# Performance work log

Hardware: AMD Instinct MI355X
Metric: run time of the kernel (lower is better)

The kernel has to match this reference:

```python
import jax, jax.numpy as jnp
import numpy as np

LEFT = 5
RIGHT = 5

def setup_inputs() -> dict:
    key = jax.random.key(0)
    k1, k2 = jax.random.split(key)
    x = jax.random.normal(k1, (32, 2000, 80), dtype=jnp.float32)
    lengths = jax.random.uniform(k2, (32,), dtype=jnp.float32)
    return {"x": x, "lengths": lengths}

def reference(x, lengths):
    # x: [B, T, C]. The torch module's grouped conv1d with a one-hot eye kernel
    # is exactly a sliding-window gather: output channel (c, i) at time t equals
    # x[t + i - LEFT, c] with zero padding outside [0, T).
    B, T, C = x.shape
    ctx_len = LEFT + RIGHT + 1
    x_pad = jnp.pad(x, ((0, 0), (LEFT, RIGHT), (0, 0)))  # [B, T+L+R, C]
    # stack shifted views: ctx[b, t, c, i] = x[t + i - LEFT, c]
    ctx = jnp.stack([x_pad[:, i:i + T, :] for i in range(ctx_len)], axis=-1)  # [B,T,C,ctx_len]
    # torch conv output channel order is channel-major (c fastest over ctx index)
    cw_x = ctx.reshape(B, T, C * ctx_len)
    # length masking: len_abs = round(T * lengths); mask[b, t] = t < len_abs[b]
    len_abs = jnp.round(T * lengths).astype(jnp.int32)
    mask = (jnp.arange(T)[None, :] < len_abs[:, None]).astype(cw_x.dtype)  # [B, T]
    return cw_x * mask[:, :, None]
```

## Files before the change

kernel.cpp:

```cpp
#include <hip/hip_runtime.h>

#define BB   32
#define TT   2000
#define CC   80
#define CTX  11
#define LEFTP 5

#define ROWQ ((CC * CTX) / 4)
#define TOTAL_Q (BB * TT * ROWQ)

__global__ __launch_bounds__(256) void context_window_kernel(
    const float* __restrict__ x,
    const float* __restrict__ lengths,
    float* __restrict__ out)
{
    int gid = blockIdx.x * blockDim.x + threadIdx.x;
    if (gid >= TOTAL_Q) return;

    int b   = gid / (TT * ROWQ);
    int rem = gid - b * (TT * ROWQ);
    int t   = rem / ROWQ;
    int q   = rem - t * ROWQ;
    int k0  = q * 4;

    int len = __float2int_rn((float)TT * lengths[b]);

    float4 v;
    if (t >= len) {
        v = make_float4(0.f, 0.f, 0.f, 0.f);
    } else {
        const float* xb = x + (size_t)b * TT * CC;
        float vals[4];
#pragma unroll
        for (int j = 0; j < 4; ++j) {
            int k  = k0 + j;
            int c  = k / CTX;
            int i  = k - c * CTX;
            int tt = t + i - LEFTP;
            vals[j] = (tt >= 0 && tt < TT) ? xb[tt * CC + c] : 0.f;
        }
        v = make_float4(vals[0], vals[1], vals[2], vals[3]);
    }

    ((float4*)out)[gid] = v;
}

extern "C" void kernel_launch(void* const* d_in, const int* in_sizes, int n_in,
                              void* d_out, int out_size, void* d_ws, size_t ws_size,
                              hipStream_t stream) {
    const float* x       = (const float*)d_in[0];
    const float* lengths = (const float*)d_in[1];
    float* out           = (float*)d_out;

    const int block = 256;
    const int grid  = (TOTAL_Q + block - 1) / block;
    context_window_kernel<<<grid, block, 0, stream>>>(x, lengths, out);
}
```

Measured before the change: 244.6 us.

## Stage input time tiles in LDS and emit sliding-window rows from shared memory

Each block now loads a 40-step time tile plus halo of the input into LDS with coalesced float4 loads, then builds the 880-wide context rows from LDS and writes them as coalesced float4 stores. Fully masked tiles skip the input load and only write zeros. This is meant to remove the redundant, scattered global gathers and per-element index divisions of the one-thread-per-float4 version. In exchange the grid is much smaller, each thread loops over 40 rows, and some threads are idle during the write phase.

Result: faster. 233.3 us (-4.6%).

```diff
diff --git a/kernel.cpp b/kernel.cpp
--- a/kernel.cpp
+++ b/kernel.cpp
@@ -1,48 +1,74 @@
 #include <hip/hip_runtime.h>
 
-#define BB   32
-#define TT   2000
-#define CC   80
-#define CTX  11
+#define BB    32
+#define TT    2000
+#define CC    80
+#define CTX   11
 #define LEFTP 5
 
-#define ROWQ ((CC * CTX) / 4)
-#define TOTAL_Q (BB * TT * ROWQ)
+#define TL    40
+#define NROWS (TL + 2 * LEFTP)
+#define S     84
+#define ROWQ  220
+#define NTILE (TT / TL)
 
 __global__ __launch_bounds__(256) void context_window_kernel(
     const float* __restrict__ x,
     const float* __restrict__ lengths,
     float* __restrict__ out)
 {
-    int gid = blockIdx.x * blockDim.x + threadIdx.x;
-    if (gid >= TOTAL_Q) return;
+    __shared__ float lds[NROWS * S];
 
-    int b   = gid / (TT * ROWQ);
-    int rem = gid - b * (TT * ROWQ);
-    int t   = rem / ROWQ;
-    int q   = rem - t * ROWQ;
-    int k0  = q * 4;
+    const int tile = blockIdx.x % NTILE;
+    const int b    = blockIdx.x / NTILE;
+    const int t0   = tile * TL;
+    const int tid  = threadIdx.x;
 
-    int len = __float2int_rn((float)TT * lengths[b]);
+    const int len = __float2int_rn((float)TT * lengths[b]);
 
-    float4 v;
-    if (t >= len) {
-        v = make_float4(0.f, 0.f, 0.f, 0.f);
-    } else {
-        const float* xb = x + (size_t)b * TT * CC;
-        float vals[4];
+    float4* outq = (float4*)out + ((size_t)b * TT + t0) * ROWQ;
+
+    if (t0 >= len) {
+        const float4 z = make_float4(0.f, 0.f, 0.f, 0.f);
+        for (int o = tid; o < TL * ROWQ; o += 256)
+            outq[o] = z;
+        return;
+    }
+
+    const float4* xb4 = (const float4*)(x + (size_t)b * TT * CC);
+    for (int idx = tid; idx < NROWS * (CC / 4); idx += 256) {
+        int r    = idx / (CC / 4);
+        int c4   = idx - r * (CC / 4);
+        int trow = t0 - LEFTP + r;
+        float4 v = make_float4(0.f, 0.f, 0.f, 0.f);
+        if (trow >= 0 && trow < TT) v = xb4[trow * (CC / 4) + c4];
+        *(float4*)&lds[r * S + c4 * 4] = v;
+    }
+    __syncthreads();
+
+    if (tid < ROWQ) {
+        const int q = tid;
+        int caddr[4];
 #pragma unroll
         for (int j = 0; j < 4; ++j) {
-            int k  = k0 + j;
-            int c  = k / CTX;
-            int i  = k - c * CTX;
-            int tt = t + i - LEFTP;
-            vals[j] = (tt >= 0 && tt < TT) ? xb[tt * CC + c] : 0.f;
+            int k = 4 * q + j;
+            int c = k / CTX;
+            int i = k - c * CTX;
+            caddr[j] = i * S + c;
         }
-        v = make_float4(vals[0], vals[1], vals[2], vals[3]);
+        float4* op = outq + q;
+        for (int tl = 0; tl < TL; ++tl, op += ROWQ) {
+            float4 v = make_float4(0.f, 0.f, 0.f, 0.f);
+            if (t0 + tl < len) {
+                const float* lp = &lds[tl * S];
+                v.x = lp[caddr[0]];
+                v.y = lp[caddr[1]];
+                v.z = lp[caddr[2]];
+                v.w = lp[caddr[3]];
+            }
+            *op = v;
+        }
     }
-
-    ((float4*)out)[gid] = v;
 }
 
 extern "C" void kernel_launch(void* const* d_in, const int* in_sizes, int n_in,
@@ -52,7 +78,6 @@
     const float* lengths = (const float*)d_in[1];
     float* out           = (float*)d_out;
 
-    const int block = 256;
-    const int grid  = (TOTAL_Q + block - 1) / block;
-    context_window_kernel<<<grid, block, 0, stream>>>(x, lengths, out);
+    const int grid = BB * NTILE;
+    context_window_kernel<<<grid, 256, 0, stream>>>(x, lengths, out);
 }
```
